# Performance work log

Measured on AMD Instinct MI355X. Metric: run time of the kernel, lower is better.

## Reference

```python
import jax, jax.numpy as jnp
import numpy as np


def setup_inputs() -> dict:
    key = jax.random.key(0)
    k1, k2, k3 = jax.random.split(key, 3)
    B, C, D, S = 16, 80, 1024, 14  # batch, num_classes, feature dim, conv size
    return {
        "batch_size": B,
        "img_feature_map": jax.random.normal(k1, (B, D, S, S), dtype=jnp.float32),
        "word_features": jax.random.normal(k2, (C, D), dtype=jnp.float32),
        "fc_a_w": jax.random.normal(k3, (D,), dtype=jnp.float32) / np.float32(np.sqrt(D)),
        "fc_a_b": jnp.zeros((), dtype=jnp.float32),
    }


def reference(batch_size, img_feature_map, word_features, fc_a_w, fc_a_b):
    # img_feature_map: [B, D, H, W] -> [B, H, W, D]
    img = jnp.transpose(img_feature_map, (0, 2, 3, 1))
    # class-wise gated feature: tanh(img * word) -> [B, H, W, C, D]
    gated = jnp.tanh(img[:, :, :, None, :] * word_features[None, None, None, :, :])
    # rank-1 linear score: [B, H, W, C]
    scores = jnp.einsum('bhwcd,d->bhwc', gated, fc_a_w) + fc_a_b
    B, H, W, C = scores.shape
    # softmax over spatial positions (H*W) per (batch, class)
    coef = jax.nn.softmax(scores.reshape(B, H * W, C), axis=1).reshape(B, H, W, C)
    # attention-weighted spatial pooling -> [B, C, D]
    return jnp.einsum('bhwc,bhwd->bcd', coef, img)
```

## Files before the change

kernel.cpp:

```cpp
#include <hip/hip_runtime.h>

#define BB 16
#define CC 80
#define DD 1024
#define HW 196
#define NSP (BB * HW)
#define NCH 8
#define DCH 128
#define CPB 8
#define NCQ (CC / CPB)
#define PG 16
#define TWO_LOG2E 2.8853900817779268f

__global__ __launch_bounds__(256) void scores_k(const float* __restrict__ img,
                                                const float* __restrict__ word,
                                                const float* __restrict__ fa,
                                                float* __restrict__ partial,
                                                float* __restrict__ imgT) {
    const int g = blockIdx.x * 256 + threadIdx.x;
    if (g >= NSP) return;
    const int b  = g / HW;
    const int hw = g - b * HW;
    const int d0 = blockIdx.y * DCH;
    const int c0 = blockIdx.z * CPB;

    const float* ip = img + ((size_t)b * DD + d0) * HW + hw;

    float p[CPB];
#pragma unroll
    for (int k = 0; k < CPB; ++k) p[k] = 0.f;

    for (int q = 0; q < DCH / 32; ++q) {
        float iv[32];
        const float* qp = ip + (size_t)q * 32 * HW;
#pragma unroll
        for (int i = 0; i < 32; ++i)
            iv[i] = qp[(size_t)i * HW];

        if (blockIdx.z == 0) {
            float4* tp = (float4*)(imgT + (size_t)g * DD + d0 + q * 32);
#pragma unroll
            for (int i = 0; i < 8; ++i)
                tp[i] = make_float4(iv[4 * i], iv[4 * i + 1], iv[4 * i + 2], iv[4 * i + 3]);
        }

#pragma unroll
        for (int i = 0; i < 32; ++i)
            iv[i] *= TWO_LOG2E;

        const float* fp = fa + d0 + q * 32;
#pragma unroll
        for (int k = 0; k < CPB; ++k) {
            const float* wp = word + (size_t)(c0 + k) * DD + d0 + q * 32;
            float p0 = 0.f, p1 = 0.f;
#pragma unroll
            for (int i = 0; i < 32; i += 2) {
                float y0 = iv[i]     * wp[i];
                float y1 = iv[i + 1] * wp[i + 1];
                float e0 = __builtin_amdgcn_exp2f(y0);
                float e1 = __builtin_amdgcn_exp2f(y1);
                float r0 = __builtin_amdgcn_rcpf(e0 + 1.f);
                float r1 = __builtin_amdgcn_rcpf(e1 + 1.f);
                p0 = fmaf(fp[i],     r0, p0);
                p1 = fmaf(fp[i + 1], r1, p1);
            }
            p[k] += p0 + p1;
        }
    }

#pragma unroll
    for (int k = 0; k < CPB; ++k)
        partial[(((size_t)b * NCH + blockIdx.y) * CC + (c0 + k)) * HW + hw]
            = (-TWO_LOG2E) * p[k];
}

__global__ __launch_bounds__(256) void softmax_k(float* __restrict__ partial) {
    const int bc = blockIdx.x;
    const int b = bc / CC, c = bc - b * CC;
    const int t = threadIdx.x;

    float x = -3.4e38f;
    if (t < HW) {
        float P = 0.f;
#pragma unroll
        for (int ch = 0; ch < NCH; ++ch)
            P += partial[(((size_t)b * NCH + ch) * CC + c) * HW + t];
        x = P;
    }

    __shared__ float rmax[4], rsum[4];
    const int wv = t >> 6;

    float m = x;
#pragma unroll
    for (int off = 32; off >= 1; off >>= 1) m = fmaxf(m, __shfl_xor(m, off, 64));
    if ((t & 63) == 0) rmax[wv] = m;
    __syncthreads();
    m = fmaxf(fmaxf(rmax[0], rmax[1]), fmaxf(rmax[2], rmax[3]));

    float e = (t < HW) ? __builtin_amdgcn_exp2f(x - m) : 0.f;
    float s = e;
#pragma unroll
    for (int off = 32; off >= 1; off >>= 1) s += __shfl_xor(s, off, 64);
    if ((t & 63) == 0) rsum[wv] = s;
    __syncthreads();
    s = rsum[0] + rsum[1] + rsum[2] + rsum[3];

    if (t < HW)
        partial[((size_t)b * NCH * CC + c) * HW + t] = e * __builtin_amdgcn_rcpf(s);
}

__global__ __launch_bounds__(256) void pool4_k(const float* __restrict__ imgT,
                                               const float* __restrict__ partial,
                                               float* __restrict__ out) {
    __shared__ float ct[PG * HW];
    const int b  = blockIdx.x;
    const int d0 = blockIdx.y * 128;
    const int cg = blockIdx.z * PG;
    const int t  = threadIdx.x;
    const int w  = t >> 6, l = t & 63;

    const float4* cs = (const float4*)(partial + ((size_t)b * NCH * CC + cg) * HW);
    float4* cd = (float4*)ct;
    for (int j = t; j < PG * HW / 4; j += 256) cd[j] = cs[j];
    __syncthreads();

    const float* ib  = imgT + (size_t)b * HW * DD + d0 + 2 * l;
    const float* cr0 = ct + (4 * w) * HW;

    float2 a0 = {0, 0}, a1 = {0, 0}, a2 = {0, 0}, a3 = {0, 0};
    for (int h = 0; h < HW; h += 4) {
        float2 i0 = *(const float2*)(ib + (size_t)(h    ) * DD);
        float2 i1 = *(const float2*)(ib + (size_t)(h + 1) * DD);
        float2 i2 = *(const float2*)(ib + (size_t)(h + 2) * DD);
        float2 i3 = *(const float2*)(ib + (size_t)(h + 3) * DD);
        float4 c0v = *(const float4*)(cr0 + h);
        float4 c1v = *(const float4*)(cr0 + HW + h);
        float4 c2v = *(const float4*)(cr0 + 2 * HW + h);
        float4 c3v = *(const float4*)(cr0 + 3 * HW + h);
#define ACC2(A, CV)                                                              \
        A.x = fmaf(CV.x, i0.x, fmaf(CV.y, i1.x, fmaf(CV.z, i2.x, fmaf(CV.w, i3.x, A.x)))); \
        A.y = fmaf(CV.x, i0.y, fmaf(CV.y, i1.y, fmaf(CV.z, i2.y, fmaf(CV.w, i3.y, A.y))));
        ACC2(a0, c0v)
        ACC2(a1, c1v)
        ACC2(a2, c2v)
        ACC2(a3, c3v)
#undef ACC2
    }

    float* ob = out + ((size_t)b * CC + cg + 4 * w) * DD + d0 + 2 * l;
    *(float2*)(ob)                  = a0;
    *(float2*)(ob + DD)             = a1;
    *(float2*)(ob + 2 * (size_t)DD) = a2;
    *(float2*)(ob + 3 * (size_t)DD) = a3;
}

extern "C" void kernel_launch(void* const* d_in, const int* in_sizes, int n_in,
                              void* d_out, int out_size, void* d_ws, size_t ws_size,
                              hipStream_t stream) {
    const float* img  = (const float*)d_in[1];
    const float* word = (const float*)d_in[2];
    const float* fa   = (const float*)d_in[3];
    float* out = (float*)d_out;

    float* partial = (float*)d_ws;
    float* imgT    = partial + (size_t)BB * NCH * CC * HW;

    scores_k<<<dim3((NSP + 255) / 256, NCH, NCQ), 256, 0, stream>>>(img, word, fa, partial, imgT);
    softmax_k<<<BB * CC, 256, 0, stream>>>(partial);
    pool4_k<<<dim3(BB, NCH, CC / PG), 256, 0, stream>>>(imgT, partial, out);
}
```

Baseline: 169.7 us.

## Use packed float2 math in scores, halve class block, widen pool grid

The scores kernel now processes 4 classes per block instead of 8, which doubles the grid along the class axis, and performs its multiply and FMA steps on 2-wide vector types so packed FP32 instructions can be used. The pooling kernel switches from 128 to 64 feature columns per block with one scalar column per lane, and preloads 28 spatial rows into registers per step. The goal is more parallelism and fewer VALU instructions. In exchange, the image is re-read more times in the scores kernel, and pooling issues narrower loads.

```diff
diff --git a/kernel.cpp b/kernel.cpp
--- a/kernel.cpp
+++ b/kernel.cpp
@@ -7,10 +7,12 @@
 #define NSP (BB * HW)
 #define NCH 8
 #define DCH 128
-#define CPB 8
+#define CPB 4
 #define NCQ (CC / CPB)
 #define PG 16
 #define TWO_LOG2E 2.8853900817779268f
+
+typedef float v2f __attribute__((ext_vector_type(2)));
 
 __global__ __launch_bounds__(256) void scores_k(const float* __restrict__ img,
                                                 const float* __restrict__ word,
@@ -26,9 +28,9 @@
 
     const float* ip = img + ((size_t)b * DD + d0) * HW + hw;
 
-    float p[CPB];
+    v2f p[CPB];
 #pragma unroll
-    for (int k = 0; k < CPB; ++k) p[k] = 0.f;
+    for (int k = 0; k < CPB; ++k) p[k] = (v2f)(0.f);
 
     for (int q = 0; q < DCH / 32; ++q) {
         float iv[32];
@@ -44,34 +46,41 @@
                 tp[i] = make_float4(iv[4 * i], iv[4 * i + 1], iv[4 * i + 2], iv[4 * i + 3]);
         }
 
+        v2f iv2[16];
 #pragma unroll
-        for (int i = 0; i < 32; ++i)
-            iv[i] *= TWO_LOG2E;
+        for (int i = 0; i < 16; ++i)
+            iv2[i] = (v2f){iv[2 * i], iv[2 * i + 1]} * (v2f)(TWO_LOG2E);
 
         const float* fp = fa + d0 + q * 32;
 #pragma unroll
         for (int k = 0; k < CPB; ++k) {
             const float* wp = word + (size_t)(c0 + k) * DD + d0 + q * 32;
-            float p0 = 0.f, p1 = 0.f;
+            v2f pa = (v2f)(0.f), pb = (v2f)(0.f);
 #pragma unroll
-            for (int i = 0; i < 32; i += 2) {
-                float y0 = iv[i]     * wp[i];
-                float y1 = iv[i + 1] * wp[i + 1];
-                float e0 = __builtin_amdgcn_exp2f(y0);
-                float e1 = __builtin_amdgcn_exp2f(y1);
-                float r0 = __builtin_amdgcn_rcpf(e0 + 1.f);
-                float r1 = __builtin_amdgcn_rcpf(e1 + 1.f);
-                p0 = fmaf(fp[i],     r0, p0);
-                p1 = fmaf(fp[i + 1], r1, p1);
+            for (int i = 0; i < 16; i += 2) {
+                v2f w0 = {wp[2 * i],     wp[2 * i + 1]};
+                v2f w1 = {wp[2 * i + 2], wp[2 * i + 3]};
+                v2f y0 = iv2[i]     * w0;
+                v2f y1 = iv2[i + 1] * w1;
+                v2f e0 = {__builtin_amdgcn_exp2f(y0.x), __builtin_amdgcn_exp2f(y0.y)};
+                v2f e1 = {__builtin_amdgcn_exp2f(y1.x), __builtin_amdgcn_exp2f(y1.y)};
+                v2f d0v = e0 + (v2f)(1.f);
+                v2f d1v = e1 + (v2f)(1.f);
+                v2f r0 = {__builtin_amdgcn_rcpf(d0v.x), __builtin_amdgcn_rcpf(d0v.y)};
+                v2f r1 = {__builtin_amdgcn_rcpf(d1v.x), __builtin_amdgcn_rcpf(d1v.y)};
+                v2f f0 = {fp[2 * i],     fp[2 * i + 1]};
+                v2f f1 = {fp[2 * i + 2], fp[2 * i + 3]};
+                pa = __builtin_elementwise_fma(f0, r0, pa);
+                pb = __builtin_elementwise_fma(f1, r1, pb);
             }
-            p[k] += p0 + p1;
+            p[k] += pa + pb;
         }
     }
 
 #pragma unroll
     for (int k = 0; k < CPB; ++k)
         partial[(((size_t)b * NCH + blockIdx.y) * CC + (c0 + k)) * HW + hw]
-            = (-TWO_LOG2E) * p[k];
+            = (-TWO_LOG2E) * (p[k].x + p[k].y);
 }
 
 __global__ __launch_bounds__(256) void softmax_k(float* __restrict__ partial) {
@@ -110,12 +119,12 @@
         partial[((size_t)b * NCH * CC + c) * HW + t] = e * __builtin_amdgcn_rcpf(s);
 }
 
-__global__ __launch_bounds__(256) void pool4_k(const float* __restrict__ imgT,
+__global__ __launch_bounds__(256) void pool6_k(const float* __restrict__ imgT,
                                                const float* __restrict__ partial,
                                                float* __restrict__ out) {
     __shared__ float ct[PG * HW];
     const int b  = blockIdx.x;
-    const int d0 = blockIdx.y * 128;
+    const int d0 = blockIdx.y * 64;
     const int cg = blockIdx.z * PG;
     const int t  = threadIdx.x;
     const int w  = t >> 6, l = t & 63;
@@ -125,34 +134,34 @@
     for (int j = t; j < PG * HW / 4; j += 256) cd[j] = cs[j];
     __syncthreads();
 
-    const float* ib  = imgT + (size_t)b * HW * DD + d0 + 2 * l;
+    const float* ib  = imgT + (size_t)b * HW * DD + d0 + l;
     const float* cr0 = ct + (4 * w) * HW;
 
-    float2 a0 = {0, 0}, a1 = {0, 0}, a2 = {0, 0}, a3 = {0, 0};
-    for (int h = 0; h < HW; h += 4) {
-        float2 i0 = *(const float2*)(ib + (size_t)(h    ) * DD);
-        float2 i1 = *(const float2*)(ib + (size_t)(h + 1) * DD);
-        float2 i2 = *(const float2*)(ib + (size_t)(h + 2) * DD);
-        float2 i3 = *(const float2*)(ib + (size_t)(h + 3) * DD);
-        float4 c0v = *(const float4*)(cr0 + h);
-        float4 c1v = *(const float4*)(cr0 + HW + h);
-        float4 c2v = *(const float4*)(cr0 + 2 * HW + h);
-        float4 c3v = *(const float4*)(cr0 + 3 * HW + h);
-#define ACC2(A, CV)                                                              \
-        A.x = fmaf(CV.x, i0.x, fmaf(CV.y, i1.x, fmaf(CV.z, i2.x, fmaf(CV.w, i3.x, A.x)))); \
-        A.y = fmaf(CV.x, i0.y, fmaf(CV.y, i1.y, fmaf(CV.z, i2.y, fmaf(CV.w, i3.y, A.y))));
-        ACC2(a0, c0v)
-        ACC2(a1, c1v)
-        ACC2(a2, c2v)
-        ACC2(a3, c3v)
-#undef ACC2
+    float a0 = 0.f, a1 = 0.f, a2 = 0.f, a3 = 0.f;
+    for (int hb = 0; hb < HW; hb += 28) {
+        float iv[28];
+#pragma unroll
+        for (int j = 0; j < 28; ++j)
+            iv[j] = ib[(size_t)(hb + j) * DD];
+#pragma unroll
+        for (int j = 0; j < 28; j += 4) {
+            const int h = hb + j;
+            float4 c0v = *(const float4*)(cr0 + h);
+            float4 c1v = *(const float4*)(cr0 + HW + h);
+            float4 c2v = *(const float4*)(cr0 + 2 * HW + h);
+            float4 c3v = *(const float4*)(cr0 + 3 * HW + h);
+            a0 = fmaf(c0v.x, iv[j], fmaf(c0v.y, iv[j+1], fmaf(c0v.z, iv[j+2], fmaf(c0v.w, iv[j+3], a0))));
+            a1 = fmaf(c1v.x, iv[j], fmaf(c1v.y, iv[j+1], fmaf(c1v.z, iv[j+2], fmaf(c1v.w, iv[j+3], a1))));
+            a2 = fmaf(c2v.x, iv[j], fmaf(c2v.y, iv[j+1], fmaf(c2v.z, iv[j+2], fmaf(c2v.w, iv[j+3], a2))));
+            a3 = fmaf(c3v.x, iv[j], fmaf(c3v.y, iv[j+1], fmaf(c3v.z, iv[j+2], fmaf(c3v.w, iv[j+3], a3))));
+        }
     }
 
-    float* ob = out + ((size_t)b * CC + cg + 4 * w) * DD + d0 + 2 * l;
-    *(float2*)(ob)                  = a0;
-    *(float2*)(ob + DD)             = a1;
-    *(float2*)(ob + 2 * (size_t)DD) = a2;
-    *(float2*)(ob + 3 * (size_t)DD) = a3;
+    float* ob = out + ((size_t)b * CC + cg + 4 * w) * DD + d0 + l;
+    ob[0]              = a0;
+    ob[DD]             = a1;
+    ob[2 * (size_t)DD] = a2;
+    ob[3 * (size_t)DD] = a3;
 }
 
 extern "C" void kernel_launch(void* const* d_in, const int* in_sizes, int n_in,
@@ -168,5 +177,5 @@
 
     scores_k<<<dim3((NSP + 255) / 256, NCH, NCQ), 256, 0, stream>>>(img, word, fa, partial, imgT);
     softmax_k<<<BB * CC, 256, 0, stream>>>(partial);
-    pool4_k<<<dim3(BB, NCH, CC / PG), 256, 0, stream>>>(imgT, partial, out);
+    pool6_k<<<dim3(BB, DD / 64, CC / PG), 256, 0, stream>>>(imgT, partial, out);
 }
```

New measurement: 154.5 us. 8.9% less time.
